# Kernel optimization log

Measured on AMD Instinct MI355X. Metric: run time of the kernel, lower is better.

The kernel has to match this reference:

```python
import jax, jax.numpy as jnp
import numpy as np

B, S, D, H = 2, 2048, 1024, 16
DK = D // H


def setup_inputs() -> dict:
    key = jax.random.key(0)
    ks = jax.random.split(key, 11)
    s = 1.0 / np.sqrt(D)
    inp = {
        "q": jax.random.normal(ks[0], (B, S, D), jnp.float32),
        "k": jax.random.normal(ks[1], (B, S, D), jnp.float32),
        "v": jax.random.normal(ks[2], (B, S, D), jnp.float32),
        "mask": jnp.tril(jnp.ones((S, S), jnp.int32))[None, None],  # [1,1,S,S] causal
        "wq": jax.random.normal(ks[3], (D, D), jnp.float32) * s,
        "bq": jax.random.normal(ks[4], (D,), jnp.float32) * s,
        "wk": jax.random.normal(ks[5], (D, D), jnp.float32) * s,
        "bk": jax.random.normal(ks[6], (D,), jnp.float32) * s,
        "wv": jax.random.normal(ks[7], (D, D), jnp.float32) * s,
        "bv": jax.random.normal(ks[8], (D,), jnp.float32) * s,
        "wo": jax.random.normal(ks[9], (D, D), jnp.float32) * s,
        "bo": jax.random.normal(ks[10], (D,), jnp.float32) * s,
    }
    return inp


def reference(q, k, v, mask, wq, bq, wk, bk, wv, bv, wo, bo):
    # Linear projections (torch Linear: x @ W.T + b)
    def split_heads(x):  # [B,S,D] -> [B,H,S,DK]
        return x.reshape(B, S, H, DK).transpose(0, 2, 1, 3)

    query = split_heads(q @ wq.T + bq)
    key_ = split_heads(k @ wk.T + bk)
    value = split_heads(v @ wv.T + bv)

    scale = 1.0 / jnp.sqrt(jnp.asarray(DK, q.dtype))
    scores = jnp.einsum("bhqd,bhkd->bhqk", query, key_) * scale
    scores = jnp.where(mask == 0, jnp.asarray(-1e9, scores.dtype), scores)
    attn = jax.nn.softmax(scores, axis=-1)  # dropout=0.0 -> identity
    x = jnp.einsum("bhqk,bhkd->bhqd", attn, value)
    x = x.transpose(0, 2, 1, 3).reshape(B, S, D)
    return x @ wo.T + bo
```

## Files before the change

### kernel.cpp

```cpp
#include <hip/hip_runtime.h>

typedef unsigned short u16;
typedef __bf16 bf16x8 __attribute__((ext_vector_type(8)));
typedef u16 u16x8 __attribute__((ext_vector_type(8)));
typedef float f32x4 __attribute__((ext_vector_type(4)));

constexpr size_t WQo = 12582912;
constexpr size_t WOo = 15728640;
constexpr size_t QPo = 16777216;
constexpr size_t KPo = 20971520;
constexpr size_t VTo = 25165824;
constexpr size_t OOo = 29360128;

#define GLD(g, l) __builtin_amdgcn_global_load_lds( \
    (const __attribute__((address_space(1))) void*)(g), \
    (__attribute__((address_space(3))) void*)(l), 16, 0, 0)

__device__ __forceinline__ u16 f2bf(float f) {
  unsigned u = __builtin_bit_cast(unsigned, f);
  u += 0x7fffu + ((u >> 16) & 1u);
  return (u16)(u >> 16);
}

__device__ __forceinline__ f32x4 zero4() {
  f32x4 z = {0.f, 0.f, 0.f, 0.f};
  return z;
}

__device__ __forceinline__ f32x4 mfma16(u16x8 a, u16x8 b, f32x4 c) {
  return __builtin_amdgcn_mfma_f32_16x16x32_bf16(
      __builtin_bit_cast(bf16x8, a), __builtin_bit_cast(bf16x8, b), c, 0, 0, 0);
}

__global__ __launch_bounds__(256) void cast_all(
    const float4* __restrict__ q, const float4* __restrict__ k, const float4* __restrict__ v,
    const float4* __restrict__ wq, const float4* __restrict__ wk,
    const float4* __restrict__ wv, const float4* __restrict__ wo,
    ushort4* __restrict__ dst)
{
  int i = blockIdx.x * 256 + threadIdx.x;
  constexpr int QN = 1048576;
  constexpr int WN = 262144;
  float4 val;
  if (i < QN)            val = q[i];
  else if (i < 2 * QN)   val = k[i - QN];
  else if (i < 3 * QN)   val = v[i - 2 * QN];
  else {
    int j = i - 3 * QN;
    if (j < WN)          val = wq[j];
    else if (j < 2 * WN) val = wk[j - WN];
    else if (j < 3 * WN) val = wv[j - 2 * WN];
    else                 val = wo[j - 3 * WN];
  }
  ushort4 o;
  o.x = f2bf(val.x); o.y = f2bf(val.y); o.z = f2bf(val.z); o.w = f2bf(val.w);
  dst[i] = o;
}

template <int TM, int BN>
__device__ __forceinline__ void gemm_core(
    const u16* __restrict__ A, const u16* __restrict__ W,
    const float* __restrict__ bias, void* __restrict__ outp,
    int m0, int n0, int mode)
{
  constexpr int Kd = 1024;
  constexpr int BM = TM * 32;
  constexpr int NJ = BN / 32;
  constexpr int AC = BM / 64;
  constexpr int BC = BN / 64;
  constexpr int ASZ = BM * 32;
  constexpr int BSZ = BN * 32;
  __shared__ alignas(16) u16 As[3 * ASZ];
  __shared__ alignas(16) u16 Bs[3 * BSZ];
  const int tid = threadIdx.x;
  const int wave = tid >> 6, lane = tid & 63;
  const int q4 = lane >> 4, l15 = lane & 15;
  const int wm = (wave >> 1) * (TM * 16), wn = (wave & 1) * (BN / 2);

  const u16* asrc[AC]; int adst[AC];
#pragma unroll
  for (int t = 0; t < AC; ++t) {
    const int pos = t * 256 + tid;
    const int lr = pos >> 3, p = pos & 7;
    const int c = p ^ (lr & 7);
    asrc[t] = A + (size_t)(m0 + lr * 2 + (c >> 2)) * Kd + (c & 3) * 8;
    adst[t] = pos * 8;
  }
  const u16* bsrc[BC]; int bdst[BC];
#pragma unroll
  for (int t = 0; t < BC; ++t) {
    const int pos = t * 256 + tid;
    const int lr = pos >> 3, p = pos & 7;
    const int c = p ^ (lr & 7);
    bsrc[t] = W + (size_t)(n0 + lr * 2 + (c >> 2)) * Kd + (c & 3) * 8;
    bdst[t] = pos * 8;
  }
  int aoff[TM], boff[NJ];
#pragma unroll
  for (int i = 0; i < TM; ++i) {
    const int m = wm + i * 16 + l15;
    const int lr = m >> 1;
    const int p = ((m & 1) * 4 + q4) ^ (lr & 7);
    aoff[i] = lr * 64 + p * 8;
  }
#pragma unroll
  for (int j = 0; j < NJ; ++j) {
    const int m = wn + j * 16 + l15;
    const int lr = m >> 1;
    const int p = ((m & 1) * 4 + q4) ^ (lr & 7);
    boff[j] = lr * 64 + p * 8;
  }

  f32x4 acc[TM][NJ];
#pragma unroll
  for (int i = 0; i < TM; ++i)
#pragma unroll
    for (int j = 0; j < NJ; ++j) acc[i][j] = zero4();

#pragma unroll
  for (int t = 0; t < AC; ++t) GLD(asrc[t], As + adst[t]);
#pragma unroll
  for (int t = 0; t < BC; ++t) GLD(bsrc[t], Bs + bdst[t]);
#pragma unroll
  for (int t = 0; t < AC; ++t) GLD(asrc[t] + 32, As + ASZ + adst[t]);
#pragma unroll
  for (int t = 0; t < BC; ++t) GLD(bsrc[t] + 32, Bs + BSZ + bdst[t]);

  int cur = 0;
  for (int it = 0; it < 32; ++it) {
    if (it < 31) {
      asm volatile("s_waitcnt vmcnt(%0)" :: "n"(AC + BC) : "memory");
    } else {
      asm volatile("s_waitcnt vmcnt(0)" ::: "memory");
    }
    __builtin_amdgcn_s_barrier();
    if (it + 2 < 32) {
      const int kt = (it + 2) * 32;
      const int ob = (cur >= 1) ? cur - 1 : 2;
#pragma unroll
      for (int t = 0; t < AC; ++t) GLD(asrc[t] + kt, As + ob * ASZ + adst[t]);
#pragma unroll
      for (int t = 0; t < BC; ++t) GLD(bsrc[t] + kt, Bs + ob * BSZ + bdst[t]);
    }
    const u16* Ab = As + cur * ASZ;
    const u16* Bb = Bs + cur * BSZ;
    u16x8 af[TM], bfv[NJ];
#pragma unroll
    for (int i = 0; i < TM; ++i) af[i] = *(const u16x8*)&Ab[aoff[i]];
#pragma unroll
    for (int j = 0; j < NJ; ++j) bfv[j] = *(const u16x8*)&Bb[boff[j]];
#pragma unroll
    for (int i = 0; i < TM; ++i)
#pragma unroll
      for (int j = 0; j < NJ; ++j)
        acc[i][j] = mfma16(af[i], bfv[j], acc[i][j]);
    cur = (cur == 2) ? 0 : cur + 1;
  }

#pragma unroll
  for (int i = 0; i < TM; ++i) {
    const int mb = m0 + wm + i * 16 + q4 * 4;
#pragma unroll
    for (int j = 0; j < NJ; ++j) {
      const int col = n0 + wn + j * 16 + l15;
      const float bsv = bias[col];
      if (mode == 1) {
        const int bb = mb >> 11, s = mb & 2047, hh = col >> 6, dk = col & 63;
        ushort4 pk;
        pk.x = f2bf(acc[i][j][0] + bsv);
        pk.y = f2bf(acc[i][j][1] + bsv);
        pk.z = f2bf(acc[i][j][2] + bsv);
        pk.w = f2bf(acc[i][j][3] + bsv);
        *(ushort4*)&((u16*)outp)[((size_t)(bb * 16 + hh) * 64 + dk) * 2048 + s] = pk;
      } else {
#pragma unroll
        for (int r = 0; r < 4; ++r) {
          const float val = acc[i][j][r] + bsv;
          const int m = mb + r;
          if (mode == 0) {
            const int bb = m >> 11, s = m & 2047, hh = col >> 6, dk = col & 63;
            ((u16*)outp)[((size_t)(bb * 16 + hh) * 2048 + s) * 64 + dk] = f2bf(val);
          } else {
            ((float*)outp)[(size_t)m * 1024 + col] = val;
          }
        }
      }
    }
  }
}

__global__ __launch_bounds__(256) void proj_gemm(
    u16* __restrict__ ws, const float* __restrict__ bq,
    const float* __restrict__ bk, const float* __restrict__ bv)
{
  const int id = blockIdx.x;
  const int z = id >> 8, rem = id & 255;
  const int bx = rem >> 5, by = rem & 31;
  const u16* A = ws + (size_t)z * 4194304;
  const u16* W = ws + WQo + (size_t)z * 1048576;
  const float* bias = (z == 0) ? bq : ((z == 1) ? bk : bv);
  u16* outp = ws + QPo + (size_t)z * 4194304;
  gemm_core<4, 128>(A, W, bias, outp, by * 128, bx * 128, (z == 2) ? 1 : 0);
}

__global__ __launch_bounds__(256) void out_gemm(
    const u16* __restrict__ ws, const float* __restrict__ bo, float* __restrict__ out)
{
  const int id = blockIdx.x;
  const int bx = id >> 6, by = id & 63;
  gemm_core<2, 128>(ws + OOo, ws + WOo, bo, out, by * 64, bx * 128, 3);
}

__global__ __launch_bounds__(256) void flash_attn(u16* __restrict__ ws)
{
  constexpr int S = 2048;
  const int id = blockIdx.x;
  const int a = id >> 5;
  const int b = 31 - a;
  const int bh = (id & 7) * 4 + ((id >> 3) & 3);
  const int bb = bh >> 4, h = bh & 15;
  const int tid = threadIdx.x;
  const int wave = tid >> 6, lane = tid & 63;
  const int q4 = lane >> 4, l15 = lane & 15;

  __shared__ u16 QsA[64 * 64];
  __shared__ u16 QsB[64 * 64];
  __shared__ u16 Ks[2][64 * 64];
  __shared__ u16 Vs[2][64 * 64];

  const u16* Qg = ws + QPo + (size_t)bh * S * 64;
  const u16* Kg = ws + KPo + (size_t)bh * S * 64;
  const u16* Vg = ws + VTo + (size_t)bh * 64 * S;
  u16* Og = ws + OOo;

  const int ch0 = wave * 128 + lane;
  const int ch1 = ch0 + 64;
  const int r0 = ch0 >> 3, c0 = (ch0 & 7) ^ (r0 & 7);
  const int r1 = ch1 >> 3, c1 = (ch1 & 7) ^ (r1 & 7);

  GLD(Qg + (size_t)(a * 64 + r0) * 64 + c0 * 8, QsA + wave * 1024);
  GLD(Qg + (size_t)(a * 64 + r1) * 64 + c1 * 8, QsA + wave * 1024 + 512);
  GLD(Qg + (size_t)(b * 64 + r0) * 64 + c0 * 8, QsB + wave * 1024);
  GLD(Qg + (size_t)(b * 64 + r1) * 64 + c1 * 8, QsB + wave * 1024 + 512);
  GLD(Kg + (size_t)r0 * 64 + c0 * 8, Ks[0] + wave * 1024);
  GLD(Kg + (size_t)r1 * 64 + c1 * 8, Ks[0] + wave * 1024 + 512);
  GLD(Vg + (size_t)r0 * S + c0 * 8, Vs[0] + wave * 1024);
  GLD(Vg + (size_t)r1 * S + c1 * 8, Vs[0] + wave * 1024 + 512);
  __syncthreads();

  u16x8 qfA[2], qfB[2];
  {
    const int row = wave * 16 + l15;
#pragma unroll
    for (int kk = 0; kk < 2; ++kk) {
      const int c = (kk * 4 + q4) ^ (row & 7);
      qfA[kk] = *(const u16x8*)&QsA[row * 64 + c * 8];
      qfB[kk] = *(const u16x8*)&QsB[row * 64 + c * 8];
    }
  }
  u16* Ps = QsA + wave * 1024;

  f32x4 oA[4], oB[4];
  float lA[4], lB[4];
#pragma unroll
  for (int j = 0; j < 4; ++j) { oA[j] = zero4(); oB[j] = zero4(); }
#pragma unroll
  for (int r = 0; r < 4; ++r) { lA[r] = 0.f; lB[r] = 0.f; }

  for (int kt = 0; kt <= b; ++kt) {
    const u16* Ksb = Ks[kt & 1];
    const u16* Vsb = Vs[kt & 1];
    if (kt < b) {
      const u16* Kt = Kg + (size_t)(kt + 1) * 64 * 64;
      u16* Kd = Ks[(kt + 1) & 1];
      u16* Vd = Vs[(kt + 1) & 1];
      GLD(Kt + (size_t)r0 * 64 + c0 * 8, Kd + wave * 1024);
      GLD(Kt + (size_t)r1 * 64 + c1 * 8, Kd + wave * 1024 + 512);
      GLD(Vg + (size_t)r0 * S + (kt + 1) * 64 + c0 * 8, Vd + wave * 1024);
      GLD(Vg + (size_t)r1 * S + (kt + 1) * 64 + c1 * 8, Vd + wave * 1024 + 512);
    }

    auto process = [&](const u16x8* qf, f32x4* o_acc, float* l_p, int qt, bool diag) {
      f32x4 sf[4];
#pragma unroll
      for (int j = 0; j < 4; ++j) {
        f32x4 z = zero4();
        const int row = j * 16 + l15;
#pragma unroll
        for (int kk = 0; kk < 2; ++kk) {
          const int c = (kk * 4 + q4) ^ (row & 7);
          z = mfma16(qf[kk], *(const u16x8*)&Ksb[row * 64 + c * 8], z);
        }
        sf[j] = z;
      }
      if (diag) {
        const int rowg0 = qt * 64 + wave * 16 + q4 * 4;
#pragma unroll
        for (int j = 0; j < 4; ++j) {
          const int colg = kt * 64 + j * 16 + l15;
#pragma unroll
          for (int r = 0; r < 4; ++r) {
            float val = sf[j][r] * 0.125f;
            if (colg > rowg0 + r) val = -__builtin_inff();
            sf[j][r] = __expf(val);
          }
        }
      } else {
#pragma unroll
        for (int j = 0; j < 4; ++j)
#pragma unroll
          for (int r = 0; r < 4; ++r)
            sf[j][r] = __expf(sf[j][r] * 0.125f);
      }
#pragma unroll
      for (int j = 0; j < 4; ++j)
#pragma unroll
        for (int r = 0; r < 4; ++r) l_p[r] += sf[j][r];

#pragma unroll
      for (int j = 0; j < 4; ++j)
#pragma unroll
        for (int r = 0; r < 4; ++r) {
          const int m = q4 * 4 + r;
          const int srow = j * 16 + l15;
          const int pos = m * 64 + (((srow >> 3) ^ (m & 7)) << 3) + (srow & 7);
          Ps[pos] = f2bf(sf[j][r]);
        }
      u16x8 pf[2];
#pragma unroll
      for (int kk = 0; kk < 2; ++kk) {
        const int c = (kk * 4 + q4) ^ (l15 & 7);
        pf[kk] = *(const u16x8*)&Ps[l15 * 64 + c * 8];
      }
#pragma unroll
      for (int j = 0; j < 4; ++j) {
        const int row = j * 16 + l15;
#pragma unroll
        for (int kk = 0; kk < 2; ++kk) {
          const int c = (kk * 4 + q4) ^ (row & 7);
          o_acc[j] = mfma16(pf[kk], *(const u16x8*)&Vsb[row * 64 + c * 8], o_acc[j]);
        }
      }
    };

    process(qfB, oB, lB, b, kt == b);
    if (kt <= a) process(qfA, oA, lA, a, kt == a);
    __syncthreads();
  }

#pragma unroll
  for (int off = 1; off < 16; off <<= 1)
#pragma unroll
    for (int r = 0; r < 4; ++r) {
      lA[r] += __shfl_xor(lA[r], off, 64);
      lB[r] += __shfl_xor(lB[r], off, 64);
    }

#pragma unroll
  for (int r = 0; r < 4; ++r) {
    const float invA = 1.f / lA[r];
    const float invB = 1.f / lB[r];
    const int sA = a * 64 + wave * 16 + q4 * 4 + r;
    const int sB = b * 64 + wave * 16 + q4 * 4 + r;
    const size_t baseA = ((size_t)(bb * 2048 + sA)) * 1024 + h * 64;
    const size_t baseB = ((size_t)(bb * 2048 + sB)) * 1024 + h * 64;
#pragma unroll
    for (int j = 0; j < 4; ++j) {
      Og[baseA + j * 16 + l15] = f2bf(oA[j][r] * invA);
      Og[baseB + j * 16 + l15] = f2bf(oB[j][r] * invB);
    }
  }
}

extern "C" void kernel_launch(void* const* d_in, const int* in_sizes, int n_in,
                              void* d_out, int out_size, void* d_ws, size_t ws_size,
                              hipStream_t stream)
{
  const float* q  = (const float*)d_in[0];
  const float* k  = (const float*)d_in[1];
  const float* v  = (const float*)d_in[2];
  const float* wq = (const float*)d_in[4];
  const float* bq = (const float*)d_in[5];
  const float* wk = (const float*)d_in[6];
  const float* bk = (const float*)d_in[7];
  const float* wv = (const float*)d_in[8];
  const float* bv = (const float*)d_in[9];
  const float* wo = (const float*)d_in[10];
  const float* bo = (const float*)d_in[11];
  u16* ws = (u16*)d_ws;
  float* out = (float*)d_out;

  cast_all<<<16384, 256, 0, stream>>>(
      (const float4*)q, (const float4*)k, (const float4*)v,
      (const float4*)wq, (const float4*)wk, (const float4*)wv, (const float4*)wo,
      (ushort4*)ws);
  proj_gemm<<<768, 256, 0, stream>>>(ws, bq, bk, bv);
  flash_attn<<<512, 256, 0, stream>>>(ws);
  out_gemm<<<512, 256, 0, stream>>>(ws, bo, out);
}
```

Before: 227.5 us.

## Triple-buffer K/V tiles in flash attention with one barrier per iteration

Moves the K/V LDS buffers from double to triple buffering and prefetches two tiles ahead, so global loads have more time to land before use. The end-of-iteration __syncthreads is replaced by a per-iteration vmcnt wait plus s_barrier placed before the next prefetch. Separate P scratch buffers are used for the A and B query tiles so their softmax staging no longer overlaps. This raises LDS use and depends on correct manual vmcnt counting, which could break ordering if the compiler emits other global loads in between.

Result: no change. 230.8 us (+1.5%).

```diff
diff --git a/kernel.cpp b/kernel.cpp
--- a/kernel.cpp
+++ b/kernel.cpp
@@ -225,8 +225,8 @@
 
   __shared__ u16 QsA[64 * 64];
   __shared__ u16 QsB[64 * 64];
-  __shared__ u16 Ks[2][64 * 64];
-  __shared__ u16 Vs[2][64 * 64];
+  __shared__ u16 Ks[3][64 * 64];
+  __shared__ u16 Vs[3][64 * 64];
 
   const u16* Qg = ws + QPo + (size_t)bh * S * 64;
   const u16* Kg = ws + KPo + (size_t)bh * S * 64;
@@ -246,7 +246,12 @@
   GLD(Kg + (size_t)r1 * 64 + c1 * 8, Ks[0] + wave * 1024 + 512);
   GLD(Vg + (size_t)r0 * S + c0 * 8, Vs[0] + wave * 1024);
   GLD(Vg + (size_t)r1 * S + c1 * 8, Vs[0] + wave * 1024 + 512);
-  __syncthreads();
+  GLD(Kg + (size_t)(64 + r0) * 64 + c0 * 8, Ks[1] + wave * 1024);
+  GLD(Kg + (size_t)(64 + r1) * 64 + c1 * 8, Ks[1] + wave * 1024 + 512);
+  GLD(Vg + (size_t)r0 * S + 64 + c0 * 8, Vs[1] + wave * 1024);
+  GLD(Vg + (size_t)r1 * S + 64 + c1 * 8, Vs[1] + wave * 1024 + 512);
+
+  asm volatile("s_waitcnt vmcnt(8)" ::: "memory");
 
   u16x8 qfA[2], qfB[2];
   {
@@ -258,7 +263,8 @@
       qfB[kk] = *(const u16x8*)&QsB[row * 64 + c * 8];
     }
   }
-  u16* Ps = QsA + wave * 1024;
+  u16* PsB = QsA + wave * 1024;
+  u16* PsA = QsB + wave * 1024;
 
   f32x4 oA[4], oB[4];
   float lA[4], lB[4];
@@ -267,20 +273,27 @@
 #pragma unroll
   for (int r = 0; r < 4; ++r) { lA[r] = 0.f; lB[r] = 0.f; }
 
+  int cur = 0;
   for (int kt = 0; kt <= b; ++kt) {
-    const u16* Ksb = Ks[kt & 1];
-    const u16* Vsb = Vs[kt & 1];
     if (kt < b) {
-      const u16* Kt = Kg + (size_t)(kt + 1) * 64 * 64;
-      u16* Kd = Ks[(kt + 1) & 1];
-      u16* Vd = Vs[(kt + 1) & 1];
-      GLD(Kt + (size_t)r0 * 64 + c0 * 8, Kd + wave * 1024);
-      GLD(Kt + (size_t)r1 * 64 + c1 * 8, Kd + wave * 1024 + 512);
-      GLD(Vg + (size_t)r0 * S + (kt + 1) * 64 + c0 * 8, Vd + wave * 1024);
-      GLD(Vg + (size_t)r1 * S + (kt + 1) * 64 + c1 * 8, Vd + wave * 1024 + 512);
-    }
-
-    auto process = [&](const u16x8* qf, f32x4* o_acc, float* l_p, int qt, bool diag) {
+      asm volatile("s_waitcnt vmcnt(4)" ::: "memory");
+    } else {
+      asm volatile("s_waitcnt vmcnt(0)" ::: "memory");
+    }
+    __builtin_amdgcn_s_barrier();
+    if (kt + 2 <= b) {
+      const int nb = (cur >= 1) ? cur - 1 : 2;
+      const u16* Kt = Kg + (size_t)(kt + 2) * 64 * 64;
+      GLD(Kt + (size_t)r0 * 64 + c0 * 8, Ks[nb] + wave * 1024);
+      GLD(Kt + (size_t)r1 * 64 + c1 * 8, Ks[nb] + wave * 1024 + 512);
+      GLD(Vg + (size_t)r0 * S + (kt + 2) * 64 + c0 * 8, Vs[nb] + wave * 1024);
+      GLD(Vg + (size_t)r1 * S + (kt + 2) * 64 + c1 * 8, Vs[nb] + wave * 1024 + 512);
+    }
+    const u16* Ksb = Ks[cur];
+    const u16* Vsb = Vs[cur];
+
+    auto process = [&](const u16x8* qf, f32x4* o_acc, float* l_p, int qt,
+                       bool diag, u16* Ps) {
       f32x4 sf[4];
 #pragma unroll
       for (int j = 0; j < 4; ++j) {
@@ -343,9 +356,9 @@
       }
     };
 
-    process(qfB, oB, lB, b, kt == b);
-    if (kt <= a) process(qfA, oA, lA, a, kt == a);
-    __syncthreads();
+    process(qfB, oB, lB, b, kt == b, PsB);
+    if (kt <= a) process(qfA, oA, lA, a, kt == a, PsA);
+    cur = (cur == 2) ? 0 : cur + 1;
   }
 
 #pragma unroll
```

## Split paired-tile flash attention into one query tile per block, heaviest first

Applied to the files above, without the earlier changes.

The attention kernel now gives each block a single 64-row query tile instead of a balanced pair of tiles (a, 31-a). The grid doubles to 1024 blocks, ordered so the longest causal tiles launch first, and the kernel carries a launch-bounds occupancy hint of 4 blocks per CU. The loop now syncs with an explicit vmcnt wait plus barrier at the top of each step instead of a __syncthreads at the end, and shared memory shrinks to one Q buffer. The aim is more parallelism and occupancy with less per-block LDS and fewer registers, at the cost of loading K/V separately for each query tile instead of sharing them across two.

After: 226.0 us. No clear change (-0.7%).

```diff
diff --git a/kernel.cpp b/kernel.cpp
--- a/kernel.cpp
+++ b/kernel.cpp
@@ -211,20 +211,18 @@
   gemm_core<2, 128>(ws + OOo, ws + WOo, bo, out, by * 64, bx * 128, 3);
 }
 
-__global__ __launch_bounds__(256) void flash_attn(u16* __restrict__ ws)
+__global__ __launch_bounds__(256, 4) void flash_attn(u16* __restrict__ ws)
 {
   constexpr int S = 2048;
   const int id = blockIdx.x;
-  const int a = id >> 5;
-  const int b = 31 - a;
+  const int t = 31 - (id >> 5);
   const int bh = (id & 7) * 4 + ((id >> 3) & 3);
   const int bb = bh >> 4, h = bh & 15;
   const int tid = threadIdx.x;
   const int wave = tid >> 6, lane = tid & 63;
   const int q4 = lane >> 4, l15 = lane & 15;
 
-  __shared__ u16 QsA[64 * 64];
-  __shared__ u16 QsB[64 * 64];
+  __shared__ u16 Qs[64 * 64];
   __shared__ u16 Ks[2][64 * 64];
   __shared__ u16 Vs[2][64 * 64];
 
@@ -238,137 +236,126 @@
   const int r0 = ch0 >> 3, c0 = (ch0 & 7) ^ (r0 & 7);
   const int r1 = ch1 >> 3, c1 = (ch1 & 7) ^ (r1 & 7);
 
-  GLD(Qg + (size_t)(a * 64 + r0) * 64 + c0 * 8, QsA + wave * 1024);
-  GLD(Qg + (size_t)(a * 64 + r1) * 64 + c1 * 8, QsA + wave * 1024 + 512);
-  GLD(Qg + (size_t)(b * 64 + r0) * 64 + c0 * 8, QsB + wave * 1024);
-  GLD(Qg + (size_t)(b * 64 + r1) * 64 + c1 * 8, QsB + wave * 1024 + 512);
+  GLD(Qg + (size_t)(t * 64 + r0) * 64 + c0 * 8, Qs + wave * 1024);
+  GLD(Qg + (size_t)(t * 64 + r1) * 64 + c1 * 8, Qs + wave * 1024 + 512);
   GLD(Kg + (size_t)r0 * 64 + c0 * 8, Ks[0] + wave * 1024);
   GLD(Kg + (size_t)r1 * 64 + c1 * 8, Ks[0] + wave * 1024 + 512);
   GLD(Vg + (size_t)r0 * S + c0 * 8, Vs[0] + wave * 1024);
   GLD(Vg + (size_t)r1 * S + c1 * 8, Vs[0] + wave * 1024 + 512);
-  __syncthreads();
-
-  u16x8 qfA[2], qfB[2];
+
+  asm volatile("s_waitcnt vmcnt(4)" ::: "memory");
+
+  u16x8 qf[2];
   {
     const int row = wave * 16 + l15;
 #pragma unroll
     for (int kk = 0; kk < 2; ++kk) {
       const int c = (kk * 4 + q4) ^ (row & 7);
-      qfA[kk] = *(const u16x8*)&QsA[row * 64 + c * 8];
-      qfB[kk] = *(const u16x8*)&QsB[row * 64 + c * 8];
-    }
-  }
-  u16* Ps = QsA + wave * 1024;
-
-  f32x4 oA[4], oB[4];
-  float lA[4], lB[4];
-#pragma unroll
-  for (int j = 0; j < 4; ++j) { oA[j] = zero4(); oB[j] = zero4(); }
-#pragma unroll
-  for (int r = 0; r < 4; ++r) { lA[r] = 0.f; lB[r] = 0.f; }
-
-  for (int kt = 0; kt <= b; ++kt) {
-    const u16* Ksb = Ks[kt & 1];
-    const u16* Vsb = Vs[kt & 1];
-    if (kt < b) {
+      qf[kk] = *(const u16x8*)&Qs[row * 64 + c * 8];
+    }
+  }
+  u16* Ps = Qs + wave * 1024;
+
+  f32x4 o_acc[4];
+  float l_p[4];
+#pragma unroll
+  for (int j = 0; j < 4; ++j) o_acc[j] = zero4();
+#pragma unroll
+  for (int r = 0; r < 4; ++r) l_p[r] = 0.f;
+
+  for (int kt = 0; kt <= t; ++kt) {
+    asm volatile("s_waitcnt vmcnt(0)" ::: "memory");
+    __builtin_amdgcn_s_barrier();
+    const int buf = kt & 1;
+    if (kt < t) {
       const u16* Kt = Kg + (size_t)(kt + 1) * 64 * 64;
-      u16* Kd = Ks[(kt + 1) & 1];
-      u16* Vd = Vs[(kt + 1) & 1];
+      u16* Kd = Ks[buf ^ 1];
+      u16* Vd = Vs[buf ^ 1];
       GLD(Kt + (size_t)r0 * 64 + c0 * 8, Kd + wave * 1024);
       GLD(Kt + (size_t)r1 * 64 + c1 * 8, Kd + wave * 1024 + 512);
       GLD(Vg + (size_t)r0 * S + (kt + 1) * 64 + c0 * 8, Vd + wave * 1024);
       GLD(Vg + (size_t)r1 * S + (kt + 1) * 64 + c1 * 8, Vd + wave * 1024 + 512);
     }
-
-    auto process = [&](const u16x8* qf, f32x4* o_acc, float* l_p, int qt, bool diag) {
-      f32x4 sf[4];
+    const u16* Ksb = Ks[buf];
+    const u16* Vsb = Vs[buf];
+    const bool diag = (kt == t);
+
+    f32x4 sf[4];
+#pragma unroll
+    for (int j = 0; j < 4; ++j) {
+      f32x4 z = zero4();
+      const int row = j * 16 + l15;
+#pragma unroll
+      for (int kk = 0; kk < 2; ++kk) {
+        const int c = (kk * 4 + q4) ^ (row & 7);
+        z = mfma16(qf[kk], *(const u16x8*)&Ksb[row * 64 + c * 8], z);
+      }
+      sf[j] = z;
+    }
+    if (diag) {
+      const int rowg0 = t * 64 + wave * 16 + q4 * 4;
 #pragma unroll
       for (int j = 0; j < 4; ++j) {
-        f32x4 z = zero4();
-        const int row = j * 16 + l15;
-#pragma unroll
-        for (int kk = 0; kk < 2; ++kk) {
-          const int c = (kk * 4 + q4) ^ (row & 7);
-          z = mfma16(qf[kk], *(const u16x8*)&Ksb[row * 64 + c * 8], z);
+        const int colg = kt * 64 + j * 16 + l15;
+#pragma unroll
+        for (int r = 0; r < 4; ++r) {
+          float val = sf[j][r] * 0.125f;
+          if (colg > rowg0 + r) val = -__builtin_inff();
+          sf[j][r] = __expf(val);
         }
-        sf[j] = z;
-      }
-      if (diag) {
-        const int rowg0 = qt * 64 + wave * 16 + q4 * 4;
-#pragma unroll
-        for (int j = 0; j < 4; ++j) {
-          const int colg = kt * 64 + j * 16 + l15;
-#pragma unroll
-          for (int r = 0; r < 4; ++r) {
-            float val = sf[j][r] * 0.125f;
-            if (colg > rowg0 + r) val = -__builtin_inff();
-            sf[j][r] = __expf(val);
-          }
-        }
-      } else {
-#pragma unroll
-        for (int j = 0; j < 4; ++j)
-#pragma unroll
-          for (int r = 0; r < 4; ++r)
-            sf[j][r] = __expf(sf[j][r] * 0.125f);
-      }
+      }
+    } else {
 #pragma unroll
       for (int j = 0; j < 4; ++j)
 #pragma unroll
-        for (int r = 0; r < 4; ++r) l_p[r] += sf[j][r];
-
-#pragma unroll
-      for (int j = 0; j < 4; ++j)
-#pragma unroll
-        for (int r = 0; r < 4; ++r) {
-          const int m = q4 * 4 + r;
-          const int srow = j * 16 + l15;
-          const int pos = m * 64 + (((srow >> 3) ^ (m & 7)) << 3) + (srow & 7);
-          Ps[pos] = f2bf(sf[j][r]);
-        }
-      u16x8 pf[2];
+        for (int r = 0; r < 4; ++r)
+          sf[j][r] = __expf(sf[j][r] * 0.125f);
+    }
+#pragma unroll
+    for (int j = 0; j < 4; ++j)
+#pragma unroll
+      for (int r = 0; r < 4; ++r) l_p[r] += sf[j][r];
+
+#pragma unroll
+    for (int j = 0; j < 4; ++j)
+#pragma unroll
+      for (int r = 0; r < 4; ++r) {
+        const int m = q4 * 4 + r;
+        const int srow = j * 16 + l15;
+        const int pos = m * 64 + (((srow >> 3) ^ (m & 7)) << 3) + (srow & 7);
+        Ps[pos] = f2bf(sf[j][r]);
+      }
+    u16x8 pf[2];
+#pragma unroll
+    for (int kk = 0; kk < 2; ++kk) {
+      const int c = (kk * 4 + q4) ^ (l15 & 7);
+      pf[kk] = *(const u16x8*)&Ps[l15 * 64 + c * 8];
+    }
+#pragma unroll
+    for (int j = 0; j < 4; ++j) {
+      const int row = j * 16 + l15;
 #pragma unroll
       for (int kk = 0; kk < 2; ++kk) {
-        const int c = (kk * 4 + q4) ^ (l15 & 7);
-        pf[kk] = *(const u16x8*)&Ps[l15 * 64 + c * 8];
-      }
-#pragma unroll
-      for (int j = 0; j < 4; ++j) {
-        const int row = j * 16 + l15;
-#pragma unroll
-        for (int kk = 0; kk < 2; ++kk) {
-          const int c = (kk * 4 + q4) ^ (row & 7);
-          o_acc[j] = mfma16(pf[kk], *(const u16x8*)&Vsb[row * 64 + c * 8], o_acc[j]);
-        }
-      }
-    };
-
-    process(qfB, oB, lB, b, kt == b);
-    if (kt <= a) process(qfA, oA, lA, a, kt == a);
-    __syncthreads();
+        const int c = (kk * 4 + q4) ^ (row & 7);
+        o_acc[j] = mfma16(pf[kk], *(const u16x8*)&Vsb[row * 64 + c * 8], o_acc[j]);
+      }
+    }
   }
 
 #pragma unroll
   for (int off = 1; off < 16; off <<= 1)
 #pragma unroll
-    for (int r = 0; r < 4; ++r) {
-      lA[r] += __shfl_xor(lA[r], off, 64);
-      lB[r] += __shfl_xor(lB[r], off, 64);
-    }
+    for (int r = 0; r < 4; ++r)
+      l_p[r] += __shfl_xor(l_p[r], off, 64);
 
 #pragma unroll
   for (int r = 0; r < 4; ++r) {
-    const float invA = 1.f / lA[r];
-    const float invB = 1.f / lB[r];
-    const int sA = a * 64 + wave * 16 + q4 * 4 + r;
-    const int sB = b * 64 + wave * 16 + q4 * 4 + r;
-    const size_t baseA = ((size_t)(bb * 2048 + sA)) * 1024 + h * 64;
-    const size_t baseB = ((size_t)(bb * 2048 + sB)) * 1024 + h * 64;
-#pragma unroll
-    for (int j = 0; j < 4; ++j) {
-      Og[baseA + j * 16 + l15] = f2bf(oA[j][r] * invA);
-      Og[baseB + j * 16 + l15] = f2bf(oB[j][r] * invB);
-    }
+    const float inv = 1.f / l_p[r];
+    const int s = t * 64 + wave * 16 + q4 * 4 + r;
+    const size_t base = ((size_t)(bb * 2048 + s)) * 1024 + h * 64;
+#pragma unroll
+    for (int j = 0; j < 4; ++j)
+      Og[base + j * 16 + l15] = f2bf(o_acc[j][r] * inv);
   }
 }
 
@@ -395,6 +382,6 @@
       (const float4*)wq, (const float4*)wk, (const float4*)wv, (const float4*)wo,
       (ushort4*)ws);
   proj_gemm<<<768, 256, 0, stream>>>(ws, bq, bk, bv);
-  flash_attn<<<512, 256, 0, stream>>>(ws);
+  flash_attn<<<1024, 256, 0, stream>>>(ws);
   out_gemm<<<512, 256, 0, stream>>>(ws, bo, out);
 }
```
